# Kernel tuning notes

Hardware: AMD Instinct MI355X
Metric: run time of the kernel (lower is better)

## Reference

```python
import jax, jax.numpy as jnp
import numpy as np

Q_STEPS, Q_TOKENS = 16, 64
KV_STEPS, KV_TOKENS = 64, 64
WINDOW = 2
TOPK = 32
DIM = 512
BATCH = 8
NUM_CONTEXTS = 2


def build_local_mask(q_steps, q_tokens, kv_steps, kv_tokens, window):
    # centers: nearest kv step for each query step
    centers = np.round(np.linspace(0, kv_steps - 1, q_steps)).astype(np.int64)
    steps = np.arange(kv_steps)
    allowed = np.abs(steps[None, :] - centers[:, None]) <= window  # [q_steps, kv_steps]
    allowed = np.repeat(np.repeat(allowed, q_tokens, axis=0), kv_tokens, axis=1)
    return jnp.where(jnp.asarray(allowed), 0.0, -jnp.inf).astype(jnp.float32)


MASK = build_local_mask(Q_STEPS, Q_TOKENS, KV_STEPS, KV_TOKENS, WINDOW)


def setup_inputs() -> dict:
    key = jax.random.key(0)
    ks = jax.random.split(key, 12)
    s = 1.0 / np.sqrt(DIM)
    return {
        "query": jax.random.normal(ks[0], (BATCH, Q_STEPS, Q_TOKENS, DIM), jnp.float32),
        "source": jax.random.normal(ks[1], (BATCH, KV_STEPS, KV_TOKENS, DIM), jnp.float32),
        "ctx1": jax.random.normal(ks[2], (BATCH, DIM), jnp.float32),
        "ctx2": jax.random.normal(ks[3], (BATCH, DIM), jnp.float32),
        "Wq": jax.random.normal(ks[4], (DIM, DIM), jnp.float32) * s,
        "bq": jnp.zeros((DIM,), jnp.float32),
        "Wk": jax.random.normal(ks[5], (DIM, DIM), jnp.float32) * s,
        "bk": jnp.zeros((DIM,), jnp.float32),
        "Wv": jax.random.normal(ks[6], (DIM, DIM), jnp.float32) * s,
        "bv": jnp.zeros((DIM,), jnp.float32),
        "Wo": jax.random.normal(ks[7], (DIM, DIM), jnp.float32) * s,
        "bo": jnp.zeros((DIM,), jnp.float32),
        "Wc": jax.random.normal(ks[8], (NUM_CONTEXTS * DIM, 2 * DIM), jnp.float32) * s,
        "bc": jnp.zeros((2 * DIM,), jnp.float32),
    }


def reference(query, source, ctx1, ctx2, Wq, bq, Wk, bk, Wv, bv, Wo, bo, Wc, bc):
    B = query.shape[0]
    # CrossScaleCondition: fuse contexts -> per-batch FiLM params gamma, beta [B, dim]
    fused = jnp.concatenate([ctx1, ctx2], axis=-1)          # [B, num_contexts*dim]
    gb = fused @ Wc + bc                                     # [B, 2*dim]
    gamma, beta = jnp.split(gb, 2, axis=-1)

    q_flat = query.reshape(B, Q_STEPS * Q_TOKENS, DIM)       # [B, Lq, d]
    src_flat = source.reshape(B, KV_STEPS * KV_TOKENS, DIM)  # [B, Lkv, d]

    q_mod = q_flat * (1.0 + gamma[:, None, :]) + beta[:, None, :]
    q = q_mod @ Wq + bq
    k = src_flat @ Wk + bk
    v = src_flat @ Wv + bv

    scores = jnp.einsum('bqd,bkd->bqk', q, k) / jnp.sqrt(jnp.float32(DIM))
    scores = scores + MASK[None]                             # local window mask

    topk_scores, topk_idx = jax.lax.top_k(scores, TOPK)      # [B, Lq, k]
    selected_v = jax.vmap(lambda vb, ib: vb[ib])(v, topk_idx)  # [B, Lq, k, d]

    attn = jax.nn.softmax(topk_scores, axis=-1)
    out = jnp.einsum('bqk,bqkd->bqd', attn, selected_v)
    out = out @ Wo + bo
    return out.reshape(B, Q_STEPS, Q_TOKENS, DIM)
```

## Files before the change

kernel.cpp:

```cpp
#include <hip/hip_runtime.h>

#define NWIN 320
#define SCORE_SCALE 0.04419417382415922f

__constant__ int CENTERS[16] = {0,4,8,13,17,21,25,29,34,38,42,46,50,55,59,63};

typedef __attribute__((ext_vector_type(8))) short v8s;
typedef __attribute__((ext_vector_type(4))) float v4f;

__device__ __forceinline__ float bflo(unsigned u) { return __uint_as_float(u << 16); }
__device__ __forceinline__ float bfhi(unsigned u) { return __uint_as_float(u & 0xffff0000u); }
__device__ __forceinline__ float bf2f(unsigned short h) { return __uint_as_float(((unsigned)h) << 16); }
__device__ __forceinline__ unsigned short f2bf(float x) {
  unsigned u = __float_as_uint(x);
  unsigned r = 0x7fffu + ((u >> 16) & 1u);
  return (unsigned short)((u + r) >> 16);
}

__device__ __forceinline__ int t64_off(int r, int k) {
  return ((r & 31) << 7) + (((((r >> 5) << 2) | (k >> 3)) ^ (r & 7)) << 4) + ((k & 7) << 1);
}
__device__ __forceinline__ int frag_off(int r, int g) {
  return ((r & 31) << 7) + (((((r >> 5) << 2) | g) ^ (r & 7)) << 4);
}

__device__ __forceinline__ void gload_lds16(const void* g, void* l) {
  __builtin_amdgcn_global_load_lds((const __attribute__((address_space(1))) unsigned int*)g,
                                   (__attribute__((address_space(3))) unsigned int*)l, 16, 0, 0);
}

__device__ __forceinline__ void cvt8pair(float4 a, float4 b, uint4& hi4, uint4& lo4) {
  float v[8] = {a.x, a.y, a.z, a.w, b.x, b.y, b.z, b.w};
  unsigned short h[8], l[8];
  #pragma unroll
  for (int e = 0; e < 8; ++e) {
    h[e] = f2bf(v[e]);
    l[e] = f2bf(v[e] - bf2f(h[e]));
  }
  hi4.x = (unsigned)h[0] | ((unsigned)h[1] << 16);
  hi4.y = (unsigned)h[2] | ((unsigned)h[3] << 16);
  hi4.z = (unsigned)h[4] | ((unsigned)h[5] << 16);
  hi4.w = (unsigned)h[6] | ((unsigned)h[7] << 16);
  lo4.x = (unsigned)l[0] | ((unsigned)l[1] << 16);
  lo4.y = (unsigned)l[2] | ((unsigned)l[3] << 16);
  lo4.z = (unsigned)l[4] | ((unsigned)l[5] << 16);
  lo4.w = (unsigned)l[6] | ((unsigned)l[7] << 16);
}

__device__ __forceinline__ uint4 cvt8hi(float4 a, float4 b) {
  uint4 r;
  r.x = (unsigned)f2bf(a.x) | ((unsigned)f2bf(a.y) << 16);
  r.y = (unsigned)f2bf(a.z) | ((unsigned)f2bf(a.w) << 16);
  r.z = (unsigned)f2bf(b.x) | ((unsigned)f2bf(b.y) << 16);
  r.w = (unsigned)f2bf(b.z) | ((unsigned)f2bf(b.w) << 16);
  return r;
}

__global__ void film_part(const float* __restrict__ ctx1, const float* __restrict__ ctx2,
                          const float* __restrict__ Wc, float* __restrict__ part)
{
  const int b = blockIdx.y, sl = blockIdx.x, j = threadIdx.x;
  const int i0 = sl * 128;
  float acc = 0.f;
  #pragma unroll 4
  for (int t = 0; t < 128; ++t) {
    const int i = i0 + t;
    const float f = (i < 512) ? ctx1[b * 512 + i] : ctx2[b * 512 + i - 512];
    acc = fmaf(f, Wc[(size_t)i * 1024 + j], acc);
  }
  part[(b * 8 + sl) * 1024 + j] = acc;
}

__global__ void film_reduce(const float* __restrict__ part, const float* __restrict__ bc,
                            float* __restrict__ gb)
{
  const int b = blockIdx.x, j = threadIdx.x;
  float acc = bc[j];
  #pragma unroll
  for (int sl = 0; sl < 8; ++sl) acc += part[(b * 8 + sl) * 1024 + j];
  gb[b * 1024 + j] = acc;
}

__global__ void u_kernel(const float* __restrict__ Wk, const float* __restrict__ bq,
                         float* __restrict__ u)
{
  const int d = blockIdx.x, lane = threadIdx.x;
  float4 a0 = *(const float4*)&Wk[(size_t)d * 512 + lane * 8];
  float4 a1 = *(const float4*)&Wk[(size_t)d * 512 + lane * 8 + 4];
  float4 c0 = *(const float4*)&bq[lane * 8];
  float4 c1 = *(const float4*)&bq[lane * 8 + 4];
  float s = a0.x*c0.x + a0.y*c0.y + a0.z*c0.z + a0.w*c0.w
          + a1.x*c1.x + a1.y*c1.y + a1.z*c1.z + a1.w*c1.w;
  #pragma unroll
  for (int off = 32; off > 0; off >>= 1) s += __shfl_xor(s, off, 64);
  if (lane == 0) u[d] = s * SCORE_SCALE;
}

__global__ __launch_bounds__(256) void wsplit_kernel(
    const float* __restrict__ Wq, const float* __restrict__ Wk,
    unsigned short* __restrict__ Wqh, unsigned short* __restrict__ Wql,
    unsigned short* __restrict__ Wkh, unsigned short* __restrict__ Wkl)
{
  const int b = blockIdx.x;
  const int mat = b >> 7;
  const float* Wsrc = mat ? Wk : Wq;
  unsigned short* Wh = mat ? Wkh : Wqh;
  unsigned short* Wl = mat ? Wkl : Wql;
  const size_t e0 = (((size_t)(b & 127) * 256) + threadIdx.x) * 8;
  float4 x0 = *(const float4*)&Wsrc[e0];
  float4 x1 = *(const float4*)&Wsrc[e0 + 4];
  uint4 h4, l4;
  cvt8pair(x0, x1, h4, l4);
  *(uint4*)&Wh[e0] = h4;
  *(uint4*)&Wl[e0] = l4;
}

__global__ __launch_bounds__(256) void gmat_mfma(
    const unsigned short* __restrict__ Wqh, const unsigned short* __restrict__ Wql,
    const unsigned short* __restrict__ Wkh, const unsigned short* __restrict__ Wkl,
    unsigned short* __restrict__ Gt)
{
  const int tid  = threadIdx.x;
  const int lane = tid & 63, l15 = lane & 15, g = lane >> 4;
  const int wave = tid >> 6;
  const int t  = ((int)blockIdx.x << 2) | wave;
  const int ti = t >> 5, tj = t & 31;
  const int ib = ti << 4, jb = tj << 4;
  const size_t arow = (size_t)(ib + l15) * 512 + (g << 3);
  const size_t brow = (size_t)(jb + l15) * 512 + (g << 3);

  v4f acc = (v4f){0.f, 0.f, 0.f, 0.f};
  #pragma unroll 4
  for (int kk = 0; kk < 16; ++kk) {
    const int kd = kk * 32;
    const v8s ah = *(const v8s*)&Wqh[arow + kd];
    const v8s al = *(const v8s*)&Wql[arow + kd];
    const v8s bh = *(const v8s*)&Wkh[brow + kd];
    const v8s bl = *(const v8s*)&Wkl[brow + kd];
    acc = __builtin_amdgcn_mfma_f32_16x16x32_bf16(ah, bh, acc, 0, 0, 0);
    acc = __builtin_amdgcn_mfma_f32_16x16x32_bf16(al, bh, acc, 0, 0, 0);
    acc = __builtin_amdgcn_mfma_f32_16x16x32_bf16(ah, bl, acc, 0, 0, 0);
  }

  #pragma unroll
  for (int k = 0; k < 4; ++k) {
    const int gi = ib + (g << 2) + k;
    const int gj = jb + l15;
    const float v = acc[k] * SCORE_SCALE;
    const unsigned short hi = f2bf(v);
    const unsigned short lo = f2bf(v - bf2f(hi));
    const int toff = t64_off(gj & 63, gi & 31);
    *(unsigned short*)((char*)Gt + ((size_t)((gi >> 5) * 8 + (gj >> 6)) << 12) + toff) = hi;
    *(unsigned short*)((char*)Gt + ((size_t)(((gi >> 5) + 16) * 8 + (gj >> 6)) << 12) + toff) = lo;
  }
}

__global__ __launch_bounds__(256) void wconv_kernel(
    const float* __restrict__ Wv, const float* __restrict__ Wo,
    unsigned short* __restrict__ Wvt, unsigned short* __restrict__ Wot)
{
  __shared__ char img[32768];
  const int ktile = blockIdx.x;
  const int mat   = blockIdx.y;
  const float* W = mat ? Wo : Wv;
  unsigned short* Dt = mat ? Wot : Wvt;
  const int tid = threadIdx.x;
  const int k  = tid >> 3;
  const int nt = tid & 7;
  #pragma unroll
  for (int e4 = 0; e4 < 16; ++e4) {
    float4 w = *(const float4*)&W[(size_t)(ktile * 32 + k) * 512 + nt * 64 + e4 * 4];
    float vv[4] = {w.x, w.y, w.z, w.w};
    #pragma unroll
    for (int c = 0; c < 4; ++c) {
      const int n = e4 * 4 + c;
      *(unsigned short*)(img + nt * 4096 + t64_off(n, k)) = f2bf(vv[c]);
    }
  }
  __syncthreads();
  const uint4* src = (const uint4*)img;
  uint4* dst = (uint4*)((char*)Dt + (size_t)ktile * 32768);
  for (int i = tid; i < 2048; i += 256) dst[i] = src[i];
}

__global__ __launch_bounds__(256) void proj_split(
    const float* __restrict__ A, const unsigned short* __restrict__ Bt,
    const float* __restrict__ bias, const float* __restrict__ gb,
    float* __restrict__ Cf)
{
  __shared__ char smem[24576];
  char* const LAh = smem;
  char* const LAl = smem + 4096;
  char* const LBh = smem + 8192;
  char* const LBl = smem + 16384;

  const int tid  = threadIdx.x;
  const int lane = tid & 63, l15 = lane & 15, g = lane >> 4;
  const int wave = tid >> 6, wm = wave >> 1, wn = wave & 1;
  const int bid = blockIdx.x;
  const int xcd = bid & 7, idx = bid >> 3;
  const int mBlk = (idx & 15) | (xcd << 4);
  const int nBlk = idx >> 4;

  const int sr = tid >> 2;
  const int sq = tid & 3;
  const size_t arow = (size_t)(mBlk * 64 + sr) * 512 + sq * 8;
  const int gbbase = ((mBlk >> 4) * 1024) + sq * 8;
  const int awoff = t64_off(sr, sq * 8);

  int aoff[2], boff[4];
  #pragma unroll
  for (int fm = 0; fm < 2; ++fm) aoff[fm] = frag_off(wm * 32 + fm * 16 + l15, g);
  #pragma unroll
  for (int fn = 0; fn < 4; ++fn) {
    const int n = wn * 64 + fn * 16 + l15;
    boff[fn] = ((n >> 6) << 12) + frag_off(n & 63, g);
  }

  v4f acc[2][4];
  #pragma unroll
  for (int fm = 0; fm < 2; ++fm)
    #pragma unroll
    for (int fn = 0; fn < 4; ++fn) acc[fm][fn] = (v4f){0.f, 0.f, 0.f, 0.f};

  for (int tk = 0; tk < 16; ++tk) {
    const int kd = tk * 32;
    {
      const char* gsh = (const char*)Bt + ((size_t)(tk * 8 + nBlk * 2) << 12) + (size_t)tid * 16;
      const char* gsl = (const char*)Bt + ((size_t)((tk + 16) * 8 + nBlk * 2) << 12) + (size_t)tid * 16;
      #pragma unroll
      for (int i = 0; i < 2; ++i) {
        gload_lds16(gsh + i * 4096, LBh + (wave << 10) + i * 4096);
        gload_lds16(gsl + i * 4096, LBl + (wave << 10) + i * 4096);
      }
    }
    {
      float4 x0 = *(const float4*)&A[arow + kd];
      float4 x1 = *(const float4*)&A[arow + kd + 4];
      float4 g0 = *(const float4*)&gb[gbbase + kd];
      float4 g1 = *(const float4*)&gb[gbbase + kd + 4];
      float4 b0 = *(const float4*)&gb[gbbase + 512 + kd];
      float4 b1 = *(const float4*)&gb[gbbase + 512 + kd + 4];
      x0.x = fmaf(x0.x, 1.f + g0.x, b0.x); x0.y = fmaf(x0.y, 1.f + g0.y, b0.y);
      x0.z = fmaf(x0.z, 1.f + g0.z, b0.z); x0.w = fmaf(x0.w, 1.f + g0.w, b0.w);
      x1.x = fmaf(x1.x, 1.f + g1.x, b1.x); x1.y = fmaf(x1.y, 1.f + g1.y, b1.y);
      x1.z = fmaf(x1.z, 1.f + g1.z, b1.z); x1.w = fmaf(x1.w, 1.f + g1.w, b1.w);
      uint4 hi4, lo4;
      cvt8pair(x0, x1, hi4, lo4);
      *(uint4*)(LAh + awoff) = hi4;
      *(uint4*)(LAl + awoff) = lo4;
    }
    __syncthreads();
    const v8s ah0 = *(const v8s*)(LAh + aoff[0]);
    const v8s ah1 = *(const v8s*)(LAh + aoff[1]);
    const v8s al0 = *(const v8s*)(LAl + aoff[0]);
    const v8s al1 = *(const v8s*)(LAl + aoff[1]);
    #pragma unroll
    for (int fn = 0; fn < 4; ++fn) {
      const v8s bh = *(const v8s*)(LBh + boff[fn]);
      const v8s bl = *(const v8s*)(LBl + boff[fn]);
      acc[0][fn] = __builtin_amdgcn_mfma_f32_16x16x32_bf16(ah0, bh, acc[0][fn], 0, 0, 0);
      acc[1][fn] = __builtin_amdgcn_mfma_f32_16x16x32_bf16(ah1, bh, acc[1][fn], 0, 0, 0);
      acc[0][fn] = __builtin_amdgcn_mfma_f32_16x16x32_bf16(al0, bh, acc[0][fn], 0, 0, 0);
      acc[1][fn] = __builtin_amdgcn_mfma_f32_16x16x32_bf16(al1, bh, acc[1][fn], 0, 0, 0);
      acc[0][fn] = __builtin_amdgcn_mfma_f32_16x16x32_bf16(ah0, bl, acc[0][fn], 0, 0, 0);
      acc[1][fn] = __builtin_amdgcn_mfma_f32_16x16x32_bf16(ah1, bl, acc[1][fn], 0, 0, 0);
    }
    __syncthreads();
  }

  #pragma unroll
  for (int fn = 0; fn < 4; ++fn) {
    const int col = nBlk * 128 + wn * 64 + fn * 16 + l15;
    const float bv = bias[col];
    #pragma unroll
    for (int fm = 0; fm < 2; ++fm) {
      const int r0 = mBlk * 64 + wm * 32 + fm * 16 + g * 4;
      #pragma unroll
      for (int k = 0; k < 4; ++k)
        Cf[(size_t)(r0 + k) * 512 + col] = acc[fm][fn][k] + bv;
    }
  }
}

__global__ __launch_bounds__(256) void proj_v(
    const float* __restrict__ A, const unsigned short* __restrict__ Bt,
    const float* __restrict__ bias, unsigned short* __restrict__ Cb)
{
  __shared__ char smem[16384];
  char* const LA = smem;
  char* const LB = smem + 8192;

  const int tid  = threadIdx.x;
  const int lane = tid & 63, l15 = lane & 15, g = lane >> 4;
  const int wave = tid >> 6, wm = wave >> 1, wn = wave & 1;
  const int bid = blockIdx.x;
  const int xcd = bid & 7, idx = bid >> 3;
  const int mBlk = (idx & 31) | (xcd << 5);
  const int nBlk = idx >> 5;

  const int sr  = tid >> 1;
  const int sq0 = (tid & 1) << 1;
  const size_t arow = (size_t)(mBlk * 128 + sr) * 512 + sq0 * 8;
  const int aw0 = ((sr >> 6) << 12) + t64_off(sr & 63, sq0 * 8);
  const int aw1 = ((sr >> 6) << 12) + t64_off(sr & 63, sq0 * 8 + 8);

  int aoff[4], boff[4];
  #pragma unroll
  for (int fm = 0; fm < 4; ++fm) {
    const int r = wm * 64 + fm * 16 + l15;
    aoff[fm] = ((r >> 6) << 12) + frag_off(r & 63, g);
  }
  #pragma unroll
  for (int fn = 0; fn < 4; ++fn) {
    const int n = wn * 64 + fn * 16 + l15;
    boff[fn] = ((n >> 6) << 12) + frag_off(n & 63, g);
  }

  v4f acc[4][4];
  #pragma unroll
  for (int fm = 0; fm < 4; ++fm)
    #pragma unroll
    for (int fn = 0; fn < 4; ++fn) acc[fm][fn] = (v4f){0.f, 0.f, 0.f, 0.f};

  for (int tk = 0; tk < 16; ++tk) {
    const int kd = tk * 32;
    {
      const char* gs = (const char*)Bt + ((size_t)tk << 15) + ((size_t)nBlk << 13) + (size_t)tid * 16;
      #pragma unroll
      for (int i = 0; i < 2; ++i)
        gload_lds16(gs + i * 4096, LB + (wave << 10) + i * 4096);
    }
    {
      float4 x0 = *(const float4*)&A[arow + kd];
      float4 x1 = *(const float4*)&A[arow + kd + 4];
      float4 x2 = *(const float4*)&A[arow + kd + 8];
      float4 x3 = *(const float4*)&A[arow + kd + 12];
      *(uint4*)(LA + aw0) = cvt8hi(x0, x1);
      *(uint4*)(LA + aw1) = cvt8hi(x2, x3);
    }
    __syncthreads();
    v8s a_[4];
    #pragma unroll
    for (int fm = 0; fm < 4; ++fm) a_[fm] = *(const v8s*)(LA + aoff[fm]);
    #pragma unroll
    for (int fn = 0; fn < 4; ++fn) {
      const v8s bb = *(const v8s*)(LB + boff[fn]);
      #pragma unroll
      for (int fm = 0; fm < 4; ++fm)
        acc[fm][fn] = __builtin_amdgcn_mfma_f32_16x16x32_bf16(a_[fm], bb, acc[fm][fn], 0, 0, 0);
    }
    __syncthreads();
  }

  #pragma unroll
  for (int fn = 0; fn < 4; ++fn) {
    const int col = nBlk * 128 + wn * 64 + fn * 16 + l15;
    const float bv = bias[col];
    #pragma unroll
    for (int fm = 0; fm < 4; ++fm) {
      const int r0 = mBlk * 128 + wm * 64 + fm * 16 + g * 4;
      #pragma unroll
      for (int k = 0; k < 4; ++k)
        Cb[(size_t)(r0 + k) * 512 + col] = f2bf(acc[fm][fn][k] + bv);
    }
  }
}

__global__ __launch_bounds__(256) void proj_o(
    const float* __restrict__ A, const unsigned short* __restrict__ Bt,
    const float* __restrict__ bias, float* __restrict__ Cf)
{
  __shared__ char smem[12288];
  char* const LA = smem;
  char* const LB = smem + 4096;

  const int tid  = threadIdx.x;
  const int lane = tid & 63, l15 = lane & 15, g = lane >> 4;
  const int wave = tid >> 6, wm = wave >> 1, wn = wave & 1;
  const int bid = blockIdx.x;
  const int xcd = bid & 7, idx = bid >> 3;
  const int mBlk = (idx & 15) | (xcd << 4);
  const int nBlk = idx >> 4;

  const int sr = tid >> 2;
  const int sq = tid & 3;
  const size_t arow = (size_t)(mBlk * 64 + sr) * 512 + sq * 8;
  const int awoff = t64_off(sr, sq * 8);

  int aoff[2], boff[4];
  #pragma unroll
  for (int fm = 0; fm < 2; ++fm) aoff[fm] = frag_off(wm * 32 + fm * 16 + l15, g);
  #pragma unroll
  for (int fn = 0; fn < 4; ++fn) {
    const int n = wn * 64 + fn * 16 + l15;
    boff[fn] = ((n >> 6) << 12) + frag_off(n & 63, g);
  }

  v4f acc[2][4];
  #pragma unroll
  for (int fm = 0; fm < 2; ++fm)
    #pragma unroll
    for (int fn = 0; fn < 4; ++fn) acc[fm][fn] = (v4f){0.f, 0.f, 0.f, 0.f};

  for (int tk = 0; tk < 16; ++tk) {
    const int kd = tk * 32;
    {
      const char* gs = (const char*)Bt + ((size_t)tk << 15) + ((size_t)nBlk << 13) + (size_t)tid * 16;
      #pragma unroll
      for (int i = 0; i < 2; ++i)
        gload_lds16(gs + i * 4096, LB + (wave << 10) + i * 4096);
    }
    {
      float4 x0 = *(const float4*)&A[arow + kd];
      float4 x1 = *(const float4*)&A[arow + kd + 4];
      *(uint4*)(LA + awoff) = cvt8hi(x0, x1);
    }
    __syncthreads();
    const v8s a0 = *(const v8s*)(LA + aoff[0]);
    const v8s a1 = *(const v8s*)(LA + aoff[1]);
    #pragma unroll
    for (int fn = 0; fn < 4; ++fn) {
      const v8s bb = *(const v8s*)(LB + boff[fn]);
      acc[0][fn] = __builtin_amdgcn_mfma_f32_16x16x32_bf16(a0, bb, acc[0][fn], 0, 0, 0);
      acc[1][fn] = __builtin_amdgcn_mfma_f32_16x16x32_bf16(a1, bb, acc[1][fn], 0, 0, 0);
    }
    __syncthreads();
  }

  #pragma unroll
  for (int fn = 0; fn < 4; ++fn) {
    const int col = nBlk * 128 + wn * 64 + fn * 16 + l15;
    const float bv = bias[col];
    #pragma unroll
    for (int fm = 0; fm < 2; ++fm) {
      const int r0 = mBlk * 64 + wm * 32 + fm * 16 + g * 4;
      #pragma unroll
      for (int k = 0; k < 4; ++k)
        Cf[(size_t)(r0 + k) * 512 + col] = acc[fm][fn][k] + bv;
    }
  }
}

__global__ __launch_bounds__(256) void scores_mfma(
    const float* __restrict__ QG, const float* __restrict__ SRC,
    float* __restrict__ S)
{
  const int bs = blockIdx.y;
  const int s = bs & 15, b = bs >> 4;
  const int c  = CENTERS[s];
  const int lo = (c - 2 > 0) ? c - 2 : 0;
  const int hi = (c + 2 < 63) ? c + 2 : 63;
  if ((int)blockIdx.x > hi - lo) return;

  __shared__ char smem[16384];
  char* const LAh = smem;
  char* const LAl = smem + 4096;
  char* const LBh = smem + 8192;
  char* const LBl = smem + 12288;

  const int tid = threadIdx.x;
  const int lane = tid & 63, l15 = lane & 15, g = lane >> 4;
  const int wave = tid >> 6, wm = wave >> 1, wn = wave & 1;
  const int qbase  = bs << 6;
  const int kvrow0 = (b << 12) + ((lo + (int)blockIdx.x) << 6);
  const int sr = tid >> 2, sq = tid & 3;
  const size_t qrow = (size_t)(qbase + sr) * 512 + sq * 8;
  const size_t krow = (size_t)(kvrow0 + sr) * 512 + sq * 8;
  const int awoff = t64_off(sr, sq * 8);

  int aoff[2], boff[2];
  #pragma unroll
  for (int f = 0; f < 2; ++f) {
    aoff[f] = frag_off(wm * 32 + f * 16 + l15, g);
    boff[f] = frag_off(wn * 32 + f * 16 + l15, g);
  }

  v4f acc[2][2];
  #pragma unroll
  for (int i = 0; i < 2; ++i)
    #pragma unroll
    for (int j = 0; j < 2; ++j) acc[i][j] = (v4f){0.f, 0.f, 0.f, 0.f};

  for (int tk = 0; tk < 16; ++tk) {
    const int kd = tk * 32;
    {
      float4 x0 = *(const float4*)&QG[qrow + kd];
      float4 x1 = *(const float4*)&QG[qrow + kd + 4];
      uint4 ahi, alo;
      cvt8pair(x0, x1, ahi, alo);
      *(uint4*)(LAh + awoff) = ahi;
      *(uint4*)(LAl + awoff) = alo;
      float4 y0 = *(const float4*)&SRC[krow + kd];
      float4 y1 = *(const float4*)&SRC[krow + kd + 4];
      uint4 bhi, blo;
      cvt8pair(y0, y1, bhi, blo);
      *(uint4*)(LBh + awoff) = bhi;
      *(uint4*)(LBl + awoff) = blo;
    }
    __syncthreads();
    const v8s a0h = *(const v8s*)(LAh + aoff[0]);
    const v8s a1h = *(const v8s*)(LAh + aoff[1]);
    const v8s a0l = *(const v8s*)(LAl + aoff[0]);
    const v8s a1l = *(const v8s*)(LAl + aoff[1]);
    const v8s b0h = *(const v8s*)(LBh + boff[0]);
    const v8s b1h = *(const v8s*)(LBh + boff[1]);
    const v8s b0l = *(const v8s*)(LBl + boff[0]);
    const v8s b1l = *(const v8s*)(LBl + boff[1]);
    acc[0][0] = __builtin_amdgcn_mfma_f32_16x16x32_bf16(a0h, b0h, acc[0][0], 0, 0, 0);
    acc[0][1] = __builtin_amdgcn_mfma_f32_16x16x32_bf16(a0h, b1h, acc[0][1], 0, 0, 0);
    acc[1][0] = __builtin_amdgcn_mfma_f32_16x16x32_bf16(a1h, b0h, acc[1][0], 0, 0, 0);
    acc[1][1] = __builtin_amdgcn_mfma_f32_16x16x32_bf16(a1h, b1h, acc[1][1], 0, 0, 0);
    acc[0][0] = __builtin_amdgcn_mfma_f32_16x16x32_bf16(a0l, b0h, acc[0][0], 0, 0, 0);
    acc[0][1] = __builtin_amdgcn_mfma_f32_16x16x32_bf16(a0l, b1h, acc[0][1], 0, 0, 0);
    acc[1][0] = __builtin_amdgcn_mfma_f32_16x16x32_bf16(a1l, b0h, acc[1][0], 0, 0, 0);
    acc[1][1] = __builtin_amdgcn_mfma_f32_16x16x32_bf16(a1l, b1h, acc[1][1], 0, 0, 0);
    acc[0][0] = __builtin_amdgcn_mfma_f32_16x16x32_bf16(a0h, b0l, acc[0][0], 0, 0, 0);
    acc[0][1] = __builtin_amdgcn_mfma_f32_16x16x32_bf16(a0h, b1l, acc[0][1], 0, 0, 0);
    acc[1][0] = __builtin_amdgcn_mfma_f32_16x16x32_bf16(a1h, b0l, acc[1][0], 0, 0, 0);
    acc[1][1] = __builtin_amdgcn_mfma_f32_16x16x32_bf16(a1h, b1l, acc[1][1], 0, 0, 0);
    __syncthreads();
  }

  #pragma unroll
  for (int fn = 0; fn < 2; ++fn) {
    const int cl = wn * 32 + fn * 16 + l15;
    const int colS = ((int)blockIdx.x << 6) + cl;
    #pragma unroll
    for (int fm = 0; fm < 2; ++fm) {
      const int r0 = qbase + wm * 32 + fm * 16 + g * 4;
      #pragma unroll
      for (int k = 0; k < 4; ++k)
        S[(size_t)(r0 + k) * NWIN + colS] = acc[fm][fn][k];
    }
  }
}

__global__ __launch_bounds__(256) void topk_pv(
    const float* __restrict__ S, const unsigned short* __restrict__ Vb,
    float* __restrict__ O)
{
  __shared__ int   sel_i[4][32];
  __shared__ float sel_p[4][32];

  const int lane = threadIdx.x & 63;
  const int wv   = threadIdx.x >> 6;
  const int b0   = blockIdx.x;
  const int grp  = (b0 & 7) + ((b0 >> 7) << 3);
  const int blk  = (b0 >> 3) & 15;
  const int row  = (((grp << 4) + blk) << 2) + wv;
  const int b    = row >> 10;
  const int s    = (row >> 6) & 15;
  const int c    = CENTERS[s];
  const int lo   = (c - 2 > 0) ? c - 2 : 0;
  const int hi   = (c + 2 < 63) ? c + 2 : 63;
  const int L    = (hi - lo + 1) << 6;
  const size_t vbase = ((size_t)b << 12) + ((size_t)lo << 6);

  const float* srow = S + (size_t)row * NWIN;
  float f[5]; unsigned uo[5];
  #pragma unroll
  for (int j = 0; j < 5; ++j) {
    const int idx = lane + (j << 6);
    const float v = (idx < L) ? srow[idx] : -__builtin_inff();
    f[j] = v;
    const unsigned fb = __float_as_uint(v);
    uo[j] = (fb & 0x80000000u) ? ~fb : (fb | 0x80000000u);
  }

  float m = f[0];
  #pragma unroll
  for (int j = 1; j < 5; ++j) m = fmaxf(m, f[j]);
  #pragma unroll
  for (int off = 32; off > 0; off >>= 1) m = fmaxf(m, __shfl_xor(m, off, 64));

  unsigned T = 0u;
  for (int bit = 31; bit >= 0; --bit) {
    const unsigned cand = T | (1u << bit);
    int cnt = 0;
    #pragma unroll
    for (int j = 0; j < 5; ++j)
      cnt += __popcll(__ballot(uo[j] >= cand));
    if (cnt >= 32) T = cand;
  }

  int base = 0;
  #pragma unroll
  for (int j = 0; j < 5; ++j) {
    const unsigned long long gm = __ballot(uo[j] > T);
    if (uo[j] > T) {
      const int rank = base + __builtin_amdgcn_mbcnt_hi(
          (unsigned)(gm >> 32), __builtin_amdgcn_mbcnt_lo((unsigned)gm, 0));
      sel_i[wv][rank] = lane + (j << 6);
      sel_p[wv][rank] = __expf(f[j] - m);
    }
    base += __popcll(gm);
  }
  #pragma unroll
  for (int j = 0; j < 5; ++j) {
    const unsigned long long em = __ballot(uo[j] == T);
    if (uo[j] == T) {
      const int er = base + __builtin_amdgcn_mbcnt_hi(
          (unsigned)(em >> 32), __builtin_amdgcn_mbcnt_lo((unsigned)em, 0));
      if (er < 32) {
        sel_i[wv][er] = lane + (j << 6);
        sel_p[wv][er] = __expf(f[j] - m);
      }
    }
    base += __popcll(em);
  }

  asm volatile("s_waitcnt lgkmcnt(0)" ::: "memory");

  const int   si = sel_i[wv][lane & 31];
  const float sp = sel_p[wv][lane & 31];
  float dp = (lane < 32) ? sp : 0.f;
  #pragma unroll
  for (int off = 32; off > 0; off >>= 1) dp += __shfl_xor(dp, off, 64);

  float oacc[8] = {0.f,0.f,0.f,0.f,0.f,0.f,0.f,0.f};
  #pragma unroll
  for (int t = 0; t < 32; ++t) {
    const int   idx_t = __builtin_amdgcn_readlane(si, t);
    const float p_t   = __uint_as_float(
        (unsigned)__builtin_amdgcn_readlane((int)__float_as_uint(sp), t));
    const unsigned short* vrow = Vb + ((vbase + (size_t)idx_t) << 9);
    #pragma unroll
    for (int e = 0; e < 4; ++e) {
      const unsigned raw = *(const unsigned*)&vrow[(lane << 1) + (e << 7)];
      oacc[2*e]     = fmaf(p_t, bflo(raw), oacc[2*e]);
      oacc[2*e + 1] = fmaf(p_t, bfhi(raw), oacc[2*e + 1]);
    }
  }

  const float inv = 1.0f / dp;
  float* orow = O + ((size_t)row << 9);
  #pragma unroll
  for (int e = 0; e < 4; ++e) {
    float2 o2 = make_float2(oacc[2*e] * inv, oacc[2*e + 1] * inv);
    *(float2*)&orow[(lane << 1) + (e << 7)] = o2;
  }
}

extern "C" void kernel_launch(void* const* d_in, const int* in_sizes, int n_in,
                              void* d_out, int out_size, void* d_ws, size_t ws_size,
                              hipStream_t stream)
{
  (void)in_sizes; (void)n_in; (void)out_size; (void)ws_size;

  const float* query  = (const float*)d_in[0];
  const float* source = (const float*)d_in[1];
  const float* ctx1   = (const float*)d_in[2];
  const float* ctx2   = (const float*)d_in[3];
  const float* Wq     = (const float*)d_in[4];
  const float* bq     = (const float*)d_in[5];
  const float* Wk     = (const float*)d_in[6];
  const float* Wv     = (const float*)d_in[8];
  const float* bv     = (const float*)d_in[9];
  const float* Wo     = (const float*)d_in[10];
  const float* bo     = (const float*)d_in[11];
  const float* Wc     = (const float*)d_in[12];
  const float* bc     = (const float*)d_in[13];
  float* out = (float*)d_out;

  char* ws = (char*)d_ws;
  float*          qg   = (float*)(ws);
  unsigned short* v    = (unsigned short*)(ws + 16777216);
  float*          S    = (float*)(ws + 50331648);
  float*          ctx  = (float*)(ws + 60817408);
  unsigned short* Gt   = (unsigned short*)(ws + 77594624);
  unsigned short* Wvt  = (unsigned short*)(ws + 78643200);
  unsigned short* Wot  = (unsigned short*)(ws + 79167488);
  float*          gb   = (float*)(ws + 79691776);
  float*          part = (float*)(ws + 79724544);
  float*          u    = (float*)(ws + 79986688);
  unsigned short* Wqh  = (unsigned short*)(ws + 79988736);
  unsigned short* Wql  = (unsigned short*)(ws + 80513024);
  unsigned short* Wkh  = (unsigned short*)(ws + 81037312);
  unsigned short* Wkl  = (unsigned short*)(ws + 81561600);

  film_part   <<<dim3(8, 8), 1024, 0, stream>>>(ctx1, ctx2, Wc, part);
  film_reduce <<<8, 1024, 0, stream>>>(part, bc, gb);
  u_kernel    <<<512, 64, 0, stream>>>(Wk, bq, u);
  wsplit_kernel<<<256, 256, 0, stream>>>(Wq, Wk, Wqh, Wql, Wkh, Wkl);
  gmat_mfma   <<<256, 256, 0, stream>>>(Wqh, Wql, Wkh, Wkl, Gt);
  wconv_kernel<<<dim3(16, 2), 256, 0, stream>>>(Wv, Wo, Wvt, Wot);

  proj_split<<<512, 256, 0, stream>>>(query, Gt, u, gb, qg);
  proj_v<<<1024, 256, 0, stream>>>(source, Wvt, bv, v);
  scores_mfma<<<dim3(5, 128), 256, 0, stream>>>(qg, source, S);
  topk_pv<<<2048, 256, 0, stream>>>(S, v, ctx);
  proj_o<<<512, 256, 0, stream>>>(ctx, Wot, bo, out);
}
```

Before: 168.2 us.

## Load proj_v operands directly from global into MFMA fragments, drop LDS staging

Rewrites the V projection GEMM so each wave reads its A rows and pre-swizzled B fragments straight from global memory into registers, removing shared memory staging and both barriers per k-step. It also drops the XCD-aware block remapping in favour of a plain mBlk/nBlk split and unrolls the k loop by two. This removes LDS traffic and synchronisation, but data that was shared across the waves in a block is now fetched redundantly from global/L2, and A reads become strided per lane.

```diff
diff --git a/kernel.cpp b/kernel.cpp
--- a/kernel.cpp
+++ b/kernel.cpp
@@ -54,6 +54,13 @@
   r.z = (unsigned)f2bf(b.x) | ((unsigned)f2bf(b.y) << 16);
   r.w = (unsigned)f2bf(b.z) | ((unsigned)f2bf(b.w) << 16);
   return r;
+}
+
+__device__ __forceinline__ v8s cvt8hi_s(float4 a, float4 b) {
+  uint4 u = cvt8hi(a, b);
+  union { uint4 u4; v8s s8; } cv;
+  cv.u4 = u;
+  return cv.s8;
 }
 
 __global__ void film_part(const float* __restrict__ ctx1, const float* __restrict__ ctx2,
@@ -287,33 +294,22 @@
     const float* __restrict__ A, const unsigned short* __restrict__ Bt,
     const float* __restrict__ bias, unsigned short* __restrict__ Cb)
 {
-  __shared__ char smem[16384];
-  char* const LA = smem;
-  char* const LB = smem + 8192;
-
   const int tid  = threadIdx.x;
   const int lane = tid & 63, l15 = lane & 15, g = lane >> 4;
   const int wave = tid >> 6, wm = wave >> 1, wn = wave & 1;
-  const int bid = blockIdx.x;
-  const int xcd = bid & 7, idx = bid >> 3;
-  const int mBlk = (idx & 31) | (xcd << 5);
-  const int nBlk = idx >> 5;
-
-  const int sr  = tid >> 1;
-  const int sq0 = (tid & 1) << 1;
-  const size_t arow = (size_t)(mBlk * 128 + sr) * 512 + sq0 * 8;
-  const int aw0 = ((sr >> 6) << 12) + t64_off(sr & 63, sq0 * 8);
-  const int aw1 = ((sr >> 6) << 12) + t64_off(sr & 63, sq0 * 8 + 8);
-
-  int aoff[4], boff[4];
-  #pragma unroll
-  for (int fm = 0; fm < 4; ++fm) {
-    const int r = wm * 64 + fm * 16 + l15;
-    aoff[fm] = ((r >> 6) << 12) + frag_off(r & 63, g);
-  }
+  const int bid  = blockIdx.x;
+  const int mBlk = bid & 255;
+  const int nBlk = bid >> 8;
+
+  size_t arow[4];
+  #pragma unroll
+  for (int fm = 0; fm < 4; ++fm)
+    arow[fm] = (size_t)(mBlk * 128 + wm * 64 + fm * 16 + l15) * 512 + (g << 3);
+
+  int boff[4];
   #pragma unroll
   for (int fn = 0; fn < 4; ++fn) {
-    const int n = wn * 64 + fn * 16 + l15;
+    const int n = nBlk * 128 + wn * 64 + fn * 16 + l15;
     boff[fn] = ((n >> 6) << 12) + frag_off(n & 63, g);
   }
 
@@ -323,34 +319,24 @@
     #pragma unroll
     for (int fn = 0; fn < 4; ++fn) acc[fm][fn] = (v4f){0.f, 0.f, 0.f, 0.f};
 
+  #pragma unroll 2
   for (int tk = 0; tk < 16; ++tk) {
     const int kd = tk * 32;
-    {
-      const char* gs = (const char*)Bt + ((size_t)tk << 15) + ((size_t)nBlk << 13) + (size_t)tid * 16;
-      #pragma unroll
-      for (int i = 0; i < 2; ++i)
-        gload_lds16(gs + i * 4096, LB + (wave << 10) + i * 4096);
-    }
-    {
-      float4 x0 = *(const float4*)&A[arow + kd];
-      float4 x1 = *(const float4*)&A[arow + kd + 4];
-      float4 x2 = *(const float4*)&A[arow + kd + 8];
-      float4 x3 = *(const float4*)&A[arow + kd + 12];
-      *(uint4*)(LA + aw0) = cvt8hi(x0, x1);
-      *(uint4*)(LA + aw1) = cvt8hi(x2, x3);
-    }
-    __syncthreads();
     v8s a_[4];
     #pragma unroll
-    for (int fm = 0; fm < 4; ++fm) a_[fm] = *(const v8s*)(LA + aoff[fm]);
+    for (int fm = 0; fm < 4; ++fm) {
+      float4 x0 = *(const float4*)&A[arow[fm] + kd];
+      float4 x1 = *(const float4*)&A[arow[fm] + kd + 4];
+      a_[fm] = cvt8hi_s(x0, x1);
+    }
+    const char* bbase = (const char*)Bt + ((size_t)tk << 15);
     #pragma unroll
     for (int fn = 0; fn < 4; ++fn) {
-      const v8s bb = *(const v8s*)(LB + boff[fn]);
+      const v8s bb = *(const v8s*)(bbase + boff[fn]);
       #pragma unroll
       for (int fm = 0; fm < 4; ++fm)
         acc[fm][fn] = __builtin_amdgcn_mfma_f32_16x16x32_bf16(a_[fm], bb, acc[fm][fn], 0, 0, 0);
     }
-    __syncthreads();
   }
 
   #pragma unroll
```

New measurement: 194.9 us. +15.9%, slower.
